# Kernel tuning notes

Measured on AMD Instinct MI355X. Metric: run time of the kernel, lower is better.

## Reference

```python
import jax, jax.numpy as jnp
import numpy as np

B, RES, C = 4, 128, 256
HW = RES * RES
H_FFT, W_FFT = RES, RES // 2 + 1
NUM_BANDS, GATE_HIDDEN = 6, 128
LN_EPS = 1e-5
FFT_NORM = 'ortho'
INIT_RANGE = 0.02


def _band_info(h_fft, w_fft, nb):
    # static radial band partition of the rFFT2 plane (matches RadialBandGate.__init__)
    yy = np.arange(h_fft, dtype=np.float32)[:, None] / max(h_fft - 1, 1)
    xx = np.arange(w_fft, dtype=np.float32)[None, :] / max(w_fft - 1, 1)
    r = np.sqrt(yy ** 2 + xx ** 2)
    r = r / (r.max() + 1e-8)
    bid = np.minimum(np.floor(r * nb), nb - 1).astype(np.int32).reshape(-1)  # (F,)
    onehot = np.zeros((bid.size, nb), dtype=np.float32)
    onehot[np.arange(bid.size), bid] = 1.0
    counts = np.maximum(onehot.sum(0), 1.0)
    return jnp.asarray(bid), jnp.asarray(onehot), jnp.asarray(counts)

BAND_ID, BAND_ONEHOT, BAND_COUNTS = _band_info(H_FFT, W_FFT, NUM_BANDS)


def setup_inputs() -> dict:
    key = jax.random.key(0)
    ks = jax.random.split(key, 16)
    return {
        'x': jax.random.normal(ks[0], (B, HW, C), jnp.float32),
        'time': jax.random.uniform(ks[1], (B,), jnp.float32),
        'w_real': jax.random.normal(ks[2], (C, C), jnp.float32) * INIT_RANGE,
        'w_imag': jax.random.normal(ks[3], (C, C), jnp.float32) * INIT_RANGE,
        'conv_w': jax.random.normal(ks[4], (C, 1, 3, 3), jnp.float32) * 0.1,  # depthwise
        'lin_w': jax.random.normal(ks[5], (C, C), jnp.float32) * 0.02,
        'lin_b': jnp.zeros((C,), jnp.float32),
        'mlp_w1': jax.random.normal(ks[6], (GATE_HIDDEN, NUM_BANDS), jnp.float32) * 0.3,
        'mlp_b1': jnp.zeros((GATE_HIDDEN,), jnp.float32),
        'mlp_w2': jax.random.normal(ks[7], (NUM_BANDS, GATE_HIDDEN), jnp.float32) * 0.1,
        'mlp_b2': jnp.zeros((NUM_BANDS,), jnp.float32),
        'norm_ww': jax.random.normal(ks[8], (C, 1), jnp.float32) * 0.02,  # ConditionalLayerNorm.weight Linear(1,dim)
        'norm_wb': jnp.ones((C,), jnp.float32),
        'norm_bw': jax.random.normal(ks[9], (C, 1), jnp.float32) * 0.02,
        'norm_bb': jnp.zeros((C,), jnp.float32),
        'kx': jnp.asarray(0.25, jnp.float32),
        'ky': jnp.asarray(0.25, jnp.float32),
    }


def _band_gate(feat, mlp_w1, mlp_b1, mlp_w2, mlp_b2):
    # feat: (B, C, F) real. scatter-add per band via one-hot matmul, mean, MLP, gather back.
    sums = jnp.einsum('bcf,fn->bcn', feat, BAND_ONEHOT)           # (B,C,NB)
    means = sums / (BAND_COUNTS + 1e-6)
    h = jax.nn.relu(jnp.einsum('bcn,hn->bch', means, mlp_w1) + mlp_b1)
    alpha_band = jax.nn.sigmoid(jnp.einsum('bch,nh->bcn', h, mlp_w2) + mlp_b2)
    return alpha_band[:, :, BAND_ID]                               # (B,C,F)


def reference(x, time, w_real, w_imag, conv_w, lin_w, lin_b,
              mlp_w1, mlp_b1, mlp_w2, mlp_b2,
              norm_ww, norm_wb, norm_bw, norm_bb, kx, ky):
    h = w = RES
    x2 = jnp.transpose(x.reshape(B, h, w, C), (0, 3, 1, 2))        # (B,C,h,w)
    Xf = jnp.fft.rfft2(x2, norm=FFT_NORM)                          # (B,C,h_fft,w_fft) complex

    # low-frequency rectangular mask (int(sigmoid(k)*dim) == floor for positive values)
    kx_i = jnp.floor(jax.nn.sigmoid(kx) * H_FFT)
    ky_i = jnp.floor(jax.nn.sigmoid(ky) * W_FFT)
    mask = ((jnp.arange(H_FFT)[:, None] < kx_i) & (jnp.arange(W_FFT)[None, :] < ky_i))
    Xf_low = Xf * mask[None, None].astype(Xf.real.dtype)

    F = H_FFT * W_FFT
    Xf_low_flat = Xf_low.reshape(B, C, F)
    W = w_real + 1j * w_imag                                       # (C,C) complex
    Xf_low_mapped = jnp.einsum('cd,bdf->bcf', W, Xf_low_flat).reshape(B, C, H_FFT, W_FFT)

    Xf_high = Xf - Xf_low
    feat_pred = jnp.abs(jnp.abs(Xf_high).reshape(B, C, F) - jnp.abs(Xf_low).reshape(B, C, F))
    alpha = _band_gate(feat_pred, mlp_w1, mlp_b1, mlp_w2, mlp_b2).reshape(B, C, H_FFT, W_FFT)

    Xf_fused = alpha * Xf_low_mapped + (1.0 - alpha) * Xf_high
    x_spec = jnp.fft.irfft2(Xf_fused, s=(h, w), norm=FFT_NORM)     # (B,C,h,w) real

    # depthwise 3x3 conv, padding=1, no bias
    xl = jax.lax.conv_general_dilated(x2, conv_w, window_strides=(1, 1), padding='SAME',
                                      feature_group_count=C,
                                      dimension_numbers=('NCHW', 'OIHW', 'NCHW'))
    # pointwise linear over channel dim
    xc = jnp.transpose((x @ lin_w.T + lin_b).reshape(B, h, w, C), (0, 3, 1, 2))

    y = jnp.transpose(x_spec + xl + xc, (0, 2, 3, 1)).reshape(B, HW, C)

    # ConditionalLayerNorm
    mean = y.mean(axis=-1, keepdims=True)
    var = (y ** 2).mean(axis=-1, keepdims=True) - mean ** 2
    yn = (y - mean) / jnp.sqrt(var + LN_EPS)
    t = time.reshape(-1, 1)                                        # (B,1)
    weight = (t @ norm_ww.T + norm_wb)[:, None, :]                 # (B,1,C)
    bias = (t @ norm_bw.T + norm_bb)[:, None, :]
    return weight * yn + bias
```

## Files before the change

### kernel.cpp

```cpp
#include <hip/hip_runtime.h>
#include <math.h>

#define B_ 4
#define C_ 256
#define RES_ 128
#define HW_ 16384
#define WF_ 65
#define F_ 8320
#define FP_ 2880

typedef __attribute__((ext_vector_type(8))) short bf16x8;
typedef __attribute__((ext_vector_type(16))) float f32x16;

__device__ __forceinline__ int brev6(int j){ return (int)(__brev((unsigned)j) >> 26); }

__device__ __forceinline__ short f2bf(float f){
  unsigned u = __float_as_uint(f);
  unsigned r = (u + 0x7FFFu + ((u>>16)&1u)) >> 16;
  return (short)r;
}

__device__ __forceinline__ bf16x8 lds_frag(const short* p){
  union { bf16x8 v; int2 d[2]; } u;
  u.d[0] = *(const int2*)p;
  u.d[1] = *(const int2*)(p+4);
  return u.v;
}
__device__ __forceinline__ void lds_store8(short* p, bf16x8 v){
  union { bf16x8 v; int2 d[2]; } u; u.v = v;
  *(int2*)p = u.d[0]; *(int2*)(p+4) = u.d[1];
}

__device__ __forceinline__ int band_of(int row, int col){
  float yy = __fdiv_rn((float)row, 127.0f);
  float xx = __fdiv_rn((float)col, 64.0f);
  float rr = __fsqrt_rn(__fadd_rn(__fmul_rn(yy,yy), __fmul_rn(xx,xx)));
  float rm = __fadd_rn(__fsqrt_rn(2.0f), 1e-8f);
  float rn = __fdiv_rn(rr, rm);
  int b = (int)floorf(__fmul_rn(rn, 6.0f));
  return b > 5 ? 5 : b;
}

__device__ __forceinline__ float sigmoidf_(float v){ return 1.0f/(1.0f+expf(-v)); }

template<int SGN>
__device__ __forceinline__ float2 wave_fft64(float2 v, const float2* stw, int lane){
  #pragma unroll
  for (int s=0; s<6; s++){
    int H = 32 >> s;
    float ox = __shfl_xor(v.x, H);
    float oy = __shfl_xor(v.y, H);
    bool hi = (lane & H) != 0;
    float2 w = stw[s];
    float ws = (SGN < 0) ? -w.y : w.y;
    float sx = v.x + ox, sy = v.y + oy;
    float dx = ox - v.x, dy = oy - v.y;
    float rx = dx*w.x - dy*ws;
    float ry = dx*ws + dy*w.x;
    v.x = hi ? rx : sx;
    v.y = hi ? ry : sy;
  }
  return v;
}

__device__ __forceinline__ void make_stage_tw(float2* stw, int lane){
  #pragma unroll
  for (int s=0; s<6; s++){
    int H = 32 >> s;
    int t = (lane & (H-1)) << s;
    float sn, cs;
    sincosf(6.283185307179586f*(float)t/64.0f, &sn, &cs);
    stw[s] = make_float2(cs, sn);
  }
}

__device__ __forceinline__ void redist2(float2 a0, float2 a1, int lane, float2& u0, float2& u1){
  int s0 = lane >> 1, s1 = s0 + 32;
  bool odd = (lane & 1) != 0;
  float t0x = __shfl(a0.x, s0), t0y = __shfl(a0.y, s0);
  float t1x = __shfl(a1.x, s0), t1y = __shfl(a1.y, s0);
  u0 = odd ? make_float2(t1x, t1y) : make_float2(t0x, t0y);
  float q0x = __shfl(a0.x, s1), q0y = __shfl(a0.y, s1);
  float q1x = __shfl(a1.x, s1), q1y = __shfl(a1.y, s1);
  u1 = odd ? make_float2(q1x, q1y) : make_float2(q0x, q0y);
}

__global__ __launch_bounds__(1024) void k_transpose(const float* __restrict__ x, float* __restrict__ x2){
  __shared__ float tile[64][65];
  int b = blockIdx.z;
  int hw0 = blockIdx.x*64, c0 = blockIdx.y*64;
  int tx = threadIdx.x, ty = threadIdx.y;
  #pragma unroll
  for (int i=0;i<4;i++){
    int hw = hw0 + ty + i*16;
    tile[ty+i*16][tx] = x[((size_t)b*HW_ + hw)*C_ + c0 + tx];
  }
  __syncthreads();
  #pragma unroll
  for (int i=0;i<4;i++){
    int c = c0 + ty + i*16;
    x2[((size_t)b*C_ + c)*HW_ + hw0 + tx] = tile[tx][ty+i*16];
  }
}

__global__ __launch_bounds__(256) void k_counts(float* __restrict__ counts, unsigned char* __restrict__ bid_t){
  int tid = threadIdx.x;
  float acc[6] = {0,0,0,0,0,0};
  for (int p = tid; p < F_; p += 256){
    int kx = p >> 7, ky = p & 127;
    int bnd = band_of(ky, kx);
    bid_t[p] = (unsigned char)bnd;
    #pragma unroll
    for (int n=0;n<6;n++) acc[n] += (bnd==n) ? 1.0f : 0.0f;
  }
  __shared__ float red[6][256];
  #pragma unroll
  for (int n=0;n<6;n++) red[n][tid] = acc[n];
  __syncthreads();
  for (int s=128; s>0; s>>=1){
    if (tid < s){
      #pragma unroll
      for (int n=0;n<6;n++) red[n][tid] += red[n][tid+s];
    }
    __syncthreads();
  }
  if (tid < 6) counts[tid] = fmaxf(red[tid][0], 1.0f);
}

__global__ __launch_bounds__(256) void k_wbf16(const float* __restrict__ wre, const float* __restrict__ wim,
                                               const float* __restrict__ lw,
                                               short* __restrict__ Wre, short* __restrict__ Wim,
                                               short* __restrict__ WL){
  int c = blockIdx.x, tid = threadIdx.x, plane = blockIdx.y;
  int idx = c*C_ + tid;
  if (plane == 0)      Wre[idx] = f2bf(wre[idx]);
  else if (plane == 1) Wim[idx] = f2bf(wim[idx]);
  else                 WL[idx]  = f2bf(lw[idx]);
}

__global__ __launch_bounds__(256) void k_fwd_rows(const float* __restrict__ x2, float2* __restrict__ X1t){
  __shared__ float2 tile[65*33];
  int tid = threadIdx.x;
  int lane = tid & 63, wv = tid >> 6;
  float2 stw[6];
  make_stage_tw(stw, lane);
  float sn128, cs128;
  sincosf(6.283185307179586f*(float)lane/128.0f, &sn128, &cs128);
  int slice = blockIdx.x >> 2;
  int r0 = (blockIdx.x & 3) * 32;
  const float* img = x2 + (size_t)slice*HW_ + (size_t)r0*128;
  #pragma unroll
  for (int i=0; i<8; i++){
    int rr = wv*8 + i;
    float2 y = *(const float2*)(img + rr*128 + lane*2);
    float2 v = wave_fft64<-1>(y, stw, lane);
    int rbk = brev6(lane);
    float2 Yk; Yk.x = __shfl(v.x, rbk); Yk.y = __shfl(v.y, rbk);
    int rbm = brev6((64 - lane) & 63);
    float2 Ym; Ym.x = __shfl(v.x, rbm); Ym.y = __shfl(v.y, rbm);
    float sx = Yk.x + Ym.x, sy = Yk.y - Ym.y;
    float dx = Yk.x - Ym.x, dy = Yk.y + Ym.y;
    tile[lane*33 + rr] = make_float2(0.5f*(sx - sn128*dx + cs128*dy),
                                     0.5f*(sy - cs128*dx - sn128*dy));
    if (lane == 0)
      tile[64*33 + rr] = make_float2(Yk.x - Yk.y, 0.0f);
  }
  __syncthreads();
  float2* dst = X1t + (size_t)slice*F_ + r0;
  for (int p = tid; p < 65*32; p += 256){
    int kx = p >> 5, rr = p & 31;
    dst[(size_t)kx*128 + rr] = tile[kx*33 + rr];
  }
}

__global__ __launch_bounds__(256) void k_fwd_cols_gate(const float2* __restrict__ X1t, float2* __restrict__ Xft,
                                                       const float* __restrict__ counts, const unsigned char* __restrict__ bid_t,
                                                       const float* __restrict__ w1, const float* __restrict__ b1,
                                                       const float* __restrict__ w2, const float* __restrict__ b2,
                                                       float* __restrict__ alpha){
  __shared__ float red[6][256];
  __shared__ float means[6], h[128];
  int tid = threadIdx.x;
  int lane = tid & 63, wv = tid >> 6;
  float2 stw[6];
  make_stage_tw(stw, lane);
  float sn128, cs128;
  sincosf(6.283185307179586f*(float)lane/128.0f, &sn128, &cs128);
  int slice = blockIdx.x;
  const float2* xin = X1t + (size_t)slice*F_;
  float2* xout = Xft + (size_t)slice*F_;
  float acc[6] = {0,0,0,0,0,0};
  for (int kx = wv; kx < 65; kx += 4){
    float4 rv = *(const float4*)(xin + (size_t)kx*128 + (lane<<1));
    float2 a0 = make_float2(rv.x, rv.y), a1 = make_float2(rv.z, rv.w);
    float2 u0, u1;
    redist2(a0, a1, lane, u0, u1);
    float2 s = make_float2(u0.x+u1.x, u0.y+u1.y);
    float ddx = u0.x-u1.x, ddy = u0.y-u1.y;
    float2 dw = make_float2(ddx*cs128 + ddy*sn128, ddy*cs128 - ddx*sn128);
    float2 v0 = wave_fft64<-1>(s, stw, lane);
    float2 v1 = wave_fft64<-1>(dw, stw, lane);
    int rb = brev6(lane);
    float ex = __shfl(v0.x, rb), ey = __shfl(v0.y, rb);
    float ox = __shfl(v1.x, rb), oy = __shfl(v1.y, rb);
    ex *= 0.0078125f; ey *= 0.0078125f;
    ox *= 0.0078125f; oy *= 0.0078125f;
    float4 wvout = make_float4(ex, ey, ox, oy);
    *(float4*)(xout + (size_t)kx*128 + (lane<<1)) = wvout;
    float me = __fsqrt_rn(ex*ex + ey*ey);
    float mo = __fsqrt_rn(ox*ox + oy*oy);
    int be = (int)bid_t[kx*128 + (lane<<1)];
    int bo = (int)bid_t[kx*128 + (lane<<1) + 1];
    #pragma unroll
    for (int n=0;n<6;n++) acc[n] += ((be==n) ? me : 0.0f) + ((bo==n) ? mo : 0.0f);
  }
  #pragma unroll
  for (int n=0;n<6;n++) red[n][tid] = acc[n];
  __syncthreads();
  for (int s=128; s>0; s>>=1){
    if (tid < s){
      #pragma unroll
      for (int n=0;n<6;n++) red[n][tid] += red[n][tid+s];
    }
    __syncthreads();
  }
  if (tid < 6) means[tid] = red[tid][0] / (counts[tid] + 1e-6f);
  __syncthreads();
  if (tid < 128){
    float hv = b1[tid];
    #pragma unroll
    for (int n=0;n<6;n++) hv += means[n]*w1[tid*6+n];
    h[tid] = fmaxf(hv, 0.0f);
  }
  __syncthreads();
  if (tid < 6){
    float o = b2[tid];
    for (int j=0;j<128;j++) o += h[j]*w2[tid*128+j];
    alpha[slice*6 + tid] = sigmoidf_(o);
  }
}

__global__ __launch_bounds__(256) void k_xt(const float2* __restrict__ Xft,
                                            short* __restrict__ XtRe, short* __restrict__ XtIm){
  __shared__ short sre[72*130];
  __shared__ short sim[72*130];
  int tid = threadIdx.x;
  int kx = blockIdx.x, d0 = blockIdx.y*128, b = blockIdx.z;
  const float2* xb = Xft + ((size_t)(b*C_ + d0))*F_ + (size_t)kx*128;
  for (int p = tid; p < 72*128; p += 256){
    int d = p / 72, ky = p - d*72;
    float2 v = xb[(size_t)d*F_ + ky];
    sre[ky*130 + d] = f2bf(v.x);
    sim[ky*130 + d] = f2bf(v.y);
  }
  __syncthreads();
  short* dre = XtRe + ((size_t)b*FP_ + (size_t)kx*72)*C_ + d0;
  short* dim_ = XtIm + ((size_t)b*FP_ + (size_t)kx*72)*C_ + d0;
  for (int p = tid; p < 72*128; p += 256){
    int ky = p >> 7, d = p & 127;
    dre[(size_t)ky*C_ + d] = sre[ky*130 + d];
    dim_[(size_t)ky*C_ + d] = sim[ky*130 + d];
  }
}

__global__ __launch_bounds__(256) void k_mix_mfma(const short* __restrict__ Wre, const short* __restrict__ Wim,
                                                  const short* __restrict__ XtRe, const short* __restrict__ XtIm,
                                                  const float* __restrict__ kxp, const float* __restrict__ kyp,
                                                  float2* __restrict__ mappedP){
  __shared__ short Are[64][36], Aim[64][36], Bre[64][36], Bim[64][36];
  int tid = threadIdx.x;
  int fp0 = blockIdx.x*64, c0 = blockIdx.y*64, b = blockIdx.z;
  int lane = tid & 63, w = tid >> 6;
  int mt = (w >> 1)*32, nt = (w & 1)*32;
  f32x16 accre = {0.f,0.f,0.f,0.f,0.f,0.f,0.f,0.f,0.f,0.f,0.f,0.f,0.f,0.f,0.f,0.f};
  f32x16 accim = {0.f,0.f,0.f,0.f,0.f,0.f,0.f,0.f,0.f,0.f,0.f,0.f,0.f,0.f,0.f,0.f};
  const short* xrb = XtRe + ((size_t)b*FP_ + fp0)*C_;
  const short* xib = XtIm + ((size_t)b*FP_ + fp0)*C_;
  int row4 = tid >> 2, part = tid & 3;
  for (int kc=0; kc<8; kc++){
    int d0 = kc*32;
    __syncthreads();
    lds_store8(&Are[row4][part*8], *(const bf16x8*)&Wre[(c0+row4)*C_ + d0 + part*8]);
    lds_store8(&Aim[row4][part*8], *(const bf16x8*)&Wim[(c0+row4)*C_ + d0 + part*8]);
    lds_store8(&Bre[row4][part*8], *(const bf16x8*)&xrb[(size_t)row4*C_ + d0 + part*8]);
    lds_store8(&Bim[row4][part*8], *(const bf16x8*)&xib[(size_t)row4*C_ + d0 + part*8]);
    __syncthreads();
    #pragma unroll
    for (int ks=0; ks<2; ks++){
      int koff = ks*16 + (lane>>5)*8;
      bf16x8 are = lds_frag(&Are[mt + (lane&31)][koff]);
      bf16x8 aim = lds_frag(&Aim[mt + (lane&31)][koff]);
      bf16x8 bre = lds_frag(&Bre[nt + (lane&31)][koff]);
      bf16x8 bim = lds_frag(&Bim[nt + (lane&31)][koff]);
      bf16x8 naim;
      { union { bf16x8 v; unsigned u[4]; } t1, t2; t1.v = aim;
        #pragma unroll
        for (int j=0;j<4;j++) t2.u[j] = t1.u[j] ^ 0x80008000u;
        naim = t2.v; }
      accre = __builtin_amdgcn_mfma_f32_32x32x16_bf16(are,  bre, accre, 0,0,0);
      accre = __builtin_amdgcn_mfma_f32_32x32x16_bf16(naim, bim, accre, 0,0,0);
      accim = __builtin_amdgcn_mfma_f32_32x32x16_bf16(are,  bim, accim, 0,0,0);
      accim = __builtin_amdgcn_mfma_f32_32x32x16_bf16(aim,  bre, accim, 0,0,0);
    }
  }
  float rowlim = floorf(sigmoidf_(kxp[0])*128.0f);
  float collim = floorf(sigmoidf_(kyp[0])*65.0f);
  int n = fp0 + nt + (lane & 31);
  int ky = n % 72, kx = n / 72;
  bool live = ((float)ky < rowlim) && ((float)kx < collim);
  #pragma unroll
  for (int reg=0; reg<16; reg++){
    int r = (reg & 3) + 8*(reg >> 2) + 4*(lane >> 5);
    int c = c0 + mt + r;
    if (live)
      mappedP[((size_t)(b*C_ + c))*FP_ + n] = make_float2(accre[reg], accim[reg]);
  }
}

__global__ __launch_bounds__(256) void k_pw_mfma(const float* __restrict__ x, const short* __restrict__ WL,
                                                  const float* __restrict__ lb, float* __restrict__ xcs){
  __shared__ short As[64][36], Bs[64][36];
  int tid = threadIdx.x;
  int hw0 = blockIdx.x*64, c0 = blockIdx.y*64, b = blockIdx.z;
  int lane = tid & 63, w = tid >> 6;
  int mt = (w >> 1)*32, nt = (w & 1)*32;
  f32x16 acc = {0.f,0.f,0.f,0.f,0.f,0.f,0.f,0.f,0.f,0.f,0.f,0.f,0.f,0.f,0.f,0.f};
  const float* xb = x + ((size_t)b*HW_ + hw0)*C_;
  int row4 = tid >> 2, part = tid & 3;
  for (int kc=0; kc<8; kc++){
    int d0 = kc*32;
    __syncthreads();
    lds_store8(&As[row4][part*8], *(const bf16x8*)&WL[(c0+row4)*C_ + d0 + part*8]);
    {
      const float* src = &xb[(size_t)row4*C_ + d0 + part*8];
      float4 va = *(const float4*)src;
      float4 vb = *(const float4*)(src+4);
      bf16x8 bv;
      bv[0]=f2bf(va.x); bv[1]=f2bf(va.y); bv[2]=f2bf(va.z); bv[3]=f2bf(va.w);
      bv[4]=f2bf(vb.x); bv[5]=f2bf(vb.y); bv[6]=f2bf(vb.z); bv[7]=f2bf(vb.w);
      lds_store8(&Bs[row4][part*8], bv);
    }
    __syncthreads();
    #pragma unroll
    for (int ks=0; ks<2; ks++){
      int koff = ks*16 + (lane>>5)*8;
      bf16x8 a  = lds_frag(&As[mt + (lane&31)][koff]);
      bf16x8 bb = lds_frag(&Bs[nt + (lane&31)][koff]);
      acc = __builtin_amdgcn_mfma_f32_32x32x16_bf16(a, bb, acc, 0,0,0);
    }
  }
  int n = hw0 + nt + (lane & 31);
  #pragma unroll
  for (int reg=0; reg<16; reg++){
    int r = (reg & 3) + 8*(reg >> 2) + 4*(lane >> 5);
    int c = c0 + mt + r;
    xcs[((size_t)(b*C_ + c))*HW_ + n] = acc[reg] + lb[c];
  }
}

__global__ __launch_bounds__(256) void k_inv_cols(float2* __restrict__ XftY, const float2* __restrict__ mappedP,
                                                  const float* __restrict__ alpha, const unsigned char* __restrict__ bid_t,
                                                  const float* __restrict__ kxp, const float* __restrict__ kyp){
  __shared__ float al[6];
  int tid = threadIdx.x;
  int lane = tid & 63, wv = tid >> 6;
  int slice = blockIdx.x;
  float2 stw[6];
  make_stage_tw(stw, lane);
  float sn128, cs128;
  sincosf(6.283185307179586f*(float)lane/128.0f, &sn128, &cs128);
  if (tid < 6) al[tid] = alpha[slice*6 + tid];
  float rowlim = floorf(sigmoidf_(kxp[0])*128.0f);
  float collim = floorf(sigmoidf_(kyp[0])*65.0f);
  __syncthreads();
  float2* xfb = XftY + (size_t)slice*F_;
  const float2* mpb = mappedP + (size_t)slice*FP_;
  for (int kx = wv; kx < 65; kx += 4){
    float4 rv = *(const float4*)(xfb + (size_t)kx*128 + (lane<<1));
    int ky0 = lane << 1;
    float a_e = al[(int)bid_t[kx*128 + ky0]];
    float a_o = al[(int)bid_t[kx*128 + ky0 + 1]];
    bool cok  = ((float)kx < collim);
    bool in_e = cok && ((float)ky0 < rowlim);
    bool in_o = cok && ((float)(ky0+1) < rowlim);
    float2 ve, vo;
    if (in_e){
      float4 mv = *(const float4*)(mpb + (size_t)kx*72 + ky0);
      ve = make_float2(mv.x*a_e, mv.y*a_e);
      vo = in_o ? make_float2(mv.z*a_o, mv.w*a_o)
                : make_float2(rv.z*(1.0f-a_o), rv.w*(1.0f-a_o));
    } else {
      ve = make_float2(rv.x*(1.0f-a_e), rv.y*(1.0f-a_e));
      vo = make_float2(rv.z*(1.0f-a_o), rv.w*(1.0f-a_o));
    }
    float2 u0, u1;
    redist2(ve, vo, lane, u0, u1);
    float2 s = make_float2(u0.x+u1.x, u0.y+u1.y);
    float ddx = u0.x-u1.x, ddy = u0.y-u1.y;
    float2 dw = make_float2(ddx*cs128 - ddy*sn128, ddx*sn128 + ddy*cs128);
    float2 v0 = wave_fft64<1>(s, stw, lane);
    float2 v1 = wave_fft64<1>(dw, stw, lane);
    int rb = brev6(lane);
    float4 outv;
    outv.x = __shfl(v0.x, rb); outv.y = __shfl(v0.y, rb);
    outv.z = __shfl(v1.x, rb); outv.w = __shfl(v1.y, rb);
    *(float4*)(xfb + (size_t)kx*128 + (lane<<1)) = outv;
  }
}

__global__ __launch_bounds__(256,6) void k_inv_rows(const float2* __restrict__ Y1t, const float* __restrict__ xcs,
                                                    const float* __restrict__ x2, const float* __restrict__ cw,
                                                    float* __restrict__ sbuf){
  __shared__ float2 ytile[65*33];
  int tid = threadIdx.x;
  int lane = tid & 63, wv = tid >> 6;
  float2 stw[6];
  make_stage_tw(stw, lane);
  float sn128, cs128;
  sincosf(6.283185307179586f*(float)lane/128.0f, &sn128, &cs128);
  int slice = blockIdx.x >> 2;
  int ch = slice & 255;
  int r0 = (blockIdx.x & 3) * 32;
  const float* img = x2 + (size_t)slice*HW_;
  int base = r0 + wv*8;
  float2 rows[10];
  #pragma unroll
  for (int i=0;i<10;i++){
    int gr = base - 1 + i;
    rows[i] = ((unsigned)gr < 128u) ? *(const float2*)(img + (size_t)gr*128 + (lane<<1))
                                    : make_float2(0.0f, 0.0f);
  }
  const float2* ysrc = Y1t + (size_t)slice*F_ + r0;
  for (int p = tid; p < 65*32; p += 256){
    int kx = p >> 5, rr = p & 31;
    ytile[kx*33 + rr] = ysrc[(size_t)kx*128 + rr];
  }
  float w9[9];
  #pragma unroll
  for (int k=0;k<9;k++) w9[k] = cw[ch*9+k];
  __syncthreads();
  size_t gbase = (size_t)slice*HW_ + (size_t)r0*128;
  #pragma unroll
  for (int i=0;i<8;i++){
    int row = wv*8 + i;
    float2 a = ytile[lane*33 + row];
    float2 b = ytile[(64-lane)*33 + row];
    if (lane == 0){ a.y = 0.0f; b.y = 0.0f; }
    float sx = a.x + b.x, sy = a.y - b.y;
    float dx = a.x - b.x, dy = a.y + b.y;
    float2 yk = make_float2(0.5f*(sx - sn128*dx - cs128*dy),
                            0.5f*(sy + cs128*dx - sn128*dy));
    float2 v = wave_fft64<1>(yk, stw, lane);
    int rbk = brev6(lane);
    float2 z; z.x = __shfl(v.x, rbk); z.y = __shfl(v.y, rbk);
    int xx = lane << 1;
    float c0 = 0.0f, c1 = 0.0f;
    #pragma unroll
    for (int dy2=0; dy2<3; dy2++){
      float2 cv = rows[i + dy2];
      float l = __shfl_up(cv.y, 1);
      if (lane == 0) l = 0.0f;
      float r = __shfl_down(cv.x, 1);
      if (lane == 63) r = 0.0f;
      c0 += l*w9[dy2*3+0] + cv.x*w9[dy2*3+1] + cv.y*w9[dy2*3+2];
      c1 += cv.x*w9[dy2*3+0] + cv.y*w9[dy2*3+1] + r*w9[dy2*3+2];
    }
    size_t g = gbase + (size_t)(row*128 + xx);
    float2 xc = *(const float2*)&xcs[g];
    float2 o;
    o.x = z.x*0.015625f + xc.x + c0;
    o.y = z.y*0.015625f + xc.y + c1;
    *(float2*)&sbuf[g] = o;
  }
}

__global__ __launch_bounds__(256) void k_stats(const float* __restrict__ sbuf, float* __restrict__ stats){
  int g = blockIdx.x*256 + threadIdx.x;
  int b = g >> 14, hw = g & 16383;
  const float* p = sbuf + (size_t)b*C_*HW_ + hw;
  float s1 = 0.0f, s2 = 0.0f;
  for (int c=0; c<C_; c++){
    float v = p[(size_t)c*HW_];
    s1 += v; s2 += v*v;
  }
  float mean = s1 * (1.0f/256.0f);
  float var  = s2 * (1.0f/256.0f) - mean*mean;
  stats[g] = mean;
  stats[65536 + g] = 1.0f / sqrtf(var + 1e-5f);
}

__global__ __launch_bounds__(256) void k_apply(const float* __restrict__ sbuf, const float* __restrict__ stats,
                                               const float* __restrict__ timev,
                                               const float* __restrict__ nww, const float* __restrict__ nwb,
                                               const float* __restrict__ nbw, const float* __restrict__ nbb,
                                               float* __restrict__ out){
  __shared__ float tile[64][65];
  __shared__ float wv[64], bv[64], mv[64], rv[64];
  int b = blockIdx.z, c0 = blockIdx.y*64, hw0 = blockIdx.x*64;
  int tid = threadIdx.x;
  if (tid < 64){
    float t = timev[b];
    int c = c0 + tid;
    wv[tid] = t*nww[c] + nwb[c];
    bv[tid] = t*nbw[c] + nbb[c];
    mv[tid] = stats[(b<<14) + hw0 + tid];
    rv[tid] = stats[65536 + (b<<14) + hw0 + tid];
  }
  #pragma unroll
  for (int q=0;q<16;q++){
    int p = tid + q*256;
    int cl = p >> 6, hwl = p & 63;
    tile[cl][hwl] = sbuf[((size_t)(b*C_+c0+cl))*HW_ + hw0 + hwl];
  }
  __syncthreads();
  #pragma unroll
  for (int q=0;q<16;q++){
    int p = tid + q*256;
    int hwl = p >> 6, cl = p & 63;
    float v = tile[cl][hwl];
    out[((size_t)(b*HW_+hw0+hwl))*C_ + c0 + cl] = wv[cl]*((v - mv[hwl])*rv[hwl]) + bv[cl];
  }
}

extern "C" void kernel_launch(void* const* d_in, const int* in_sizes, int n_in,
                              void* d_out, int out_size, void* d_ws, size_t ws_size,
                              hipStream_t stream){
  const float* x      = (const float*)d_in[0];
  const float* timev  = (const float*)d_in[1];
  const float* w_real = (const float*)d_in[2];
  const float* w_imag = (const float*)d_in[3];
  const float* conv_w = (const float*)d_in[4];
  const float* lin_w  = (const float*)d_in[5];
  const float* lin_b  = (const float*)d_in[6];
  const float* mlp_w1 = (const float*)d_in[7];
  const float* mlp_b1 = (const float*)d_in[8];
  const float* mlp_w2 = (const float*)d_in[9];
  const float* mlp_b2 = (const float*)d_in[10];
  const float* norm_ww= (const float*)d_in[11];
  const float* norm_wb= (const float*)d_in[12];
  const float* norm_bw= (const float*)d_in[13];
  const float* norm_bb= (const float*)d_in[14];
  const float* kxp    = (const float*)d_in[15];
  const float* kyp    = (const float*)d_in[16];

  float* ws = (float*)d_ws;
  float*  alpha  = ws;
  unsigned char* bid_t = (unsigned char*)(ws + 6144);
  float*  counts = ws + 8224;
  float*  stats  = ws + 8288;
  short*  Wre_bf = (short*)(ws + 139360);
  short*  Wim_bf = (short*)(ws + 172128);
  short*  WL_bf  = (short*)(ws + 204896);
  float*  x2     = ws + 237664;
  float2* Xft    = (float2*)(ws + 17014880);
  float*  CbF    = ws + 34054240;
  float2* X1t    = (float2*)CbF;
  short*  XtRe   = (short*)CbF;
  short*  XtIm   = (short*)(CbF + 1474560);
  float2* mappedP= (float2*)(CbF + 2949120);
  float*  sb     = CbF;
  float*  xcs    = (float*)d_out;
  float*  out    = (float*)d_out;

  k_transpose    <<<dim3(256, 4, B_), dim3(64,16), 0, stream>>>(x, x2);
  k_counts       <<<1, 256, 0, stream>>>(counts, bid_t);
  k_wbf16        <<<dim3(256, 3), 256, 0, stream>>>(w_real, w_imag, lin_w, Wre_bf, Wim_bf, WL_bf);
  k_fwd_rows     <<<4096, 256, 0, stream>>>(x2, X1t);
  k_fwd_cols_gate<<<1024, 256, 0, stream>>>(X1t, Xft, counts, bid_t, mlp_w1, mlp_b1, mlp_w2, mlp_b2, alpha);
  k_xt           <<<dim3(40, 2, B_), 256, 0, stream>>>(Xft, XtRe, XtIm);
  k_pw_mfma      <<<dim3(256, 4, B_), 256, 0, stream>>>(x, WL_bf, lin_b, xcs);
  k_mix_mfma     <<<dim3(45, 4, B_), 256, 0, stream>>>(Wre_bf, Wim_bf, XtRe, XtIm, kxp, kyp, mappedP);
  k_inv_cols     <<<1024, 256, 0, stream>>>(Xft, mappedP, alpha, bid_t, kxp, kyp);
  k_inv_rows     <<<4096, 256, 0, stream>>>((const float2*)Xft, xcs, x2, conv_w, sb);
  k_stats        <<<256, 256, 0, stream>>>(sb, stats);
  k_apply        <<<dim3(256, 4, B_), 256, 0, stream>>>(sb, stats, timev, norm_ww, norm_wb, norm_bw, norm_bb, out);
}
```

Measured before the change: 430.6 us.

## Fuse LayerNorm stats into apply, vectorize transposes, warp-reduce gate sums

```diff
diff --git a/kernel.cpp b/kernel.cpp
--- a/kernel.cpp
+++ b/kernel.cpp
@@ -85,21 +85,25 @@
   u1 = odd ? make_float2(q1x, q1y) : make_float2(q0x, q0y);
 }
 
-__global__ __launch_bounds__(1024) void k_transpose(const float* __restrict__ x, float* __restrict__ x2){
-  __shared__ float tile[64][65];
+__global__ __launch_bounds__(256) void k_transpose(const float* __restrict__ x, float* __restrict__ x2){
+  __shared__ float tile[64][68];
   int b = blockIdx.z;
   int hw0 = blockIdx.x*64, c0 = blockIdx.y*64;
-  int tx = threadIdx.x, ty = threadIdx.y;
-  #pragma unroll
-  for (int i=0;i<4;i++){
-    int hw = hw0 + ty + i*16;
-    tile[ty+i*16][tx] = x[((size_t)b*HW_ + hw)*C_ + c0 + tx];
-  }
-  __syncthreads();
-  #pragma unroll
-  for (int i=0;i<4;i++){
-    int c = c0 + ty + i*16;
-    x2[((size_t)b*C_ + c)*HW_ + hw0 + tx] = tile[tx][ty+i*16];
+  int tid = threadIdx.x;
+  #pragma unroll
+  for (int q=0;q<4;q++){
+    int p = tid + q*256;
+    int hw = p >> 4, c4 = (p & 15) << 2;
+    float4 v = *(const float4*)&x[((size_t)b*HW_ + hw0 + hw)*C_ + c0 + c4];
+    *(float4*)&tile[hw][c4] = v;
+  }
+  __syncthreads();
+  #pragma unroll
+  for (int q=0;q<4;q++){
+    int p = tid + q*256;
+    int c = p >> 4, h4 = (p & 15) << 2;
+    float4 v = make_float4(tile[h4][c], tile[h4+1][c], tile[h4+2][c], tile[h4+3][c]);
+    *(float4*)&x2[((size_t)b*C_ + c0 + c)*HW_ + hw0 + h4] = v;
   }
 }
 
@@ -167,9 +171,10 @@
   }
   __syncthreads();
   float2* dst = X1t + (size_t)slice*F_ + r0;
-  for (int p = tid; p < 65*32; p += 256){
-    int kx = p >> 5, rr = p & 31;
-    dst[(size_t)kx*128 + rr] = tile[kx*33 + rr];
+  for (int p = tid; p < 65*16; p += 256){
+    int kx = p >> 4, r2 = (p & 15) << 1;
+    float2 a = tile[kx*33 + r2], b = tile[kx*33 + r2 + 1];
+    *(float4*)(dst + (size_t)kx*128 + r2) = make_float4(a.x, a.y, b.x, b.y);
   }
 }
 
@@ -178,7 +183,7 @@
                                                        const float* __restrict__ w1, const float* __restrict__ b1,
                                                        const float* __restrict__ w2, const float* __restrict__ b2,
                                                        float* __restrict__ alpha){
-  __shared__ float red[6][256];
+  __shared__ float red[6][4];
   __shared__ float means[6], h[128];
   int tid = threadIdx.x;
   int lane = tid & 63, wv = tid >> 6;
@@ -215,16 +220,14 @@
     for (int n=0;n<6;n++) acc[n] += ((be==n) ? me : 0.0f) + ((bo==n) ? mo : 0.0f);
   }
   #pragma unroll
-  for (int n=0;n<6;n++) red[n][tid] = acc[n];
-  __syncthreads();
-  for (int s=128; s>0; s>>=1){
-    if (tid < s){
-      #pragma unroll
-      for (int n=0;n<6;n++) red[n][tid] += red[n][tid+s];
-    }
-    __syncthreads();
-  }
-  if (tid < 6) means[tid] = red[tid][0] / (counts[tid] + 1e-6f);
+  for (int n=0;n<6;n++){
+    float v = acc[n];
+    #pragma unroll
+    for (int off=32; off>0; off>>=1) v += __shfl_xor(v, off);
+    if (lane == 0) red[n][wv] = v;
+  }
+  __syncthreads();
+  if (tid < 6) means[tid] = (red[tid][0]+red[tid][1]+red[tid][2]+red[tid][3]) / (counts[tid] + 1e-6f);
   __syncthreads();
   if (tid < 128){
     float hv = b1[tid];
@@ -408,7 +411,7 @@
   }
 }
 
-__global__ __launch_bounds__(256,6) void k_inv_rows(const float2* __restrict__ Y1t, const float* __restrict__ xcs,
+__global__ __launch_bounds__(256,8) void k_inv_rows(const float2* __restrict__ Y1t, const float* __restrict__ xcs,
                                                     const float* __restrict__ x2, const float* __restrict__ cw,
                                                     float* __restrict__ sbuf){
   __shared__ float2 ytile[65*33];
@@ -431,9 +434,11 @@
                                     : make_float2(0.0f, 0.0f);
   }
   const float2* ysrc = Y1t + (size_t)slice*F_ + r0;
-  for (int p = tid; p < 65*32; p += 256){
-    int kx = p >> 5, rr = p & 31;
-    ytile[kx*33 + rr] = ysrc[(size_t)kx*128 + rr];
+  for (int p = tid; p < 65*16; p += 256){
+    int kx = p >> 4, r2 = (p & 15) << 1;
+    float4 v = *(const float4*)(ysrc + (size_t)kx*128 + r2);
+    ytile[kx*33 + r2]     = make_float2(v.x, v.y);
+    ytile[kx*33 + r2 + 1] = make_float2(v.z, v.w);
   }
   float w9[9];
   #pragma unroll
@@ -474,51 +479,55 @@
   }
 }
 
-__global__ __launch_bounds__(256) void k_stats(const float* __restrict__ sbuf, float* __restrict__ stats){
-  int g = blockIdx.x*256 + threadIdx.x;
-  int b = g >> 14, hw = g & 16383;
-  const float* p = sbuf + (size_t)b*C_*HW_ + hw;
+__global__ __launch_bounds__(256) void k_norm(const float* __restrict__ sbuf, const float* __restrict__ timev,
+                                              const float* __restrict__ nww, const float* __restrict__ nwb,
+                                              const float* __restrict__ nbw, const float* __restrict__ nbb,
+                                              float* __restrict__ out){
+  __shared__ float tile[64][65];
+  __shared__ float p1[64][5], p2[64][5];
+  __shared__ float mv[64], rv[64], wv_[256], bv_[256];
+  int b = blockIdx.y, hw0 = blockIdx.x*64;
+  int tid = threadIdx.x;
+  {
+    float t = timev[b];
+    wv_[tid] = t*nww[tid] + nwb[tid];
+    bv_[tid] = t*nbw[tid] + nbb[tid];
+  }
+  int hwl = tid & 63, cg = tid >> 6;
+  const float* p = sbuf + (size_t)b*C_*HW_ + hw0 + hwl;
   float s1 = 0.0f, s2 = 0.0f;
-  for (int c=0; c<C_; c++){
+  for (int c = cg*64; c < cg*64 + 64; c++){
     float v = p[(size_t)c*HW_];
     s1 += v; s2 += v*v;
   }
-  float mean = s1 * (1.0f/256.0f);
-  float var  = s2 * (1.0f/256.0f) - mean*mean;
-  stats[g] = mean;
-  stats[65536 + g] = 1.0f / sqrtf(var + 1e-5f);
-}
-
-__global__ __launch_bounds__(256) void k_apply(const float* __restrict__ sbuf, const float* __restrict__ stats,
-                                               const float* __restrict__ timev,
-                                               const float* __restrict__ nww, const float* __restrict__ nwb,
-                                               const float* __restrict__ nbw, const float* __restrict__ nbb,
-                                               float* __restrict__ out){
-  __shared__ float tile[64][65];
-  __shared__ float wv[64], bv[64], mv[64], rv[64];
-  int b = blockIdx.z, c0 = blockIdx.y*64, hw0 = blockIdx.x*64;
-  int tid = threadIdx.x;
+  p1[hwl][cg] = s1; p2[hwl][cg] = s2;
+  __syncthreads();
   if (tid < 64){
-    float t = timev[b];
-    int c = c0 + tid;
-    wv[tid] = t*nww[c] + nwb[c];
-    bv[tid] = t*nbw[c] + nbb[c];
-    mv[tid] = stats[(b<<14) + hw0 + tid];
-    rv[tid] = stats[65536 + (b<<14) + hw0 + tid];
-  }
-  #pragma unroll
-  for (int q=0;q<16;q++){
-    int p = tid + q*256;
-    int cl = p >> 6, hwl = p & 63;
-    tile[cl][hwl] = sbuf[((size_t)(b*C_+c0+cl))*HW_ + hw0 + hwl];
-  }
-  __syncthreads();
-  #pragma unroll
-  for (int q=0;q<16;q++){
-    int p = tid + q*256;
-    int hwl = p >> 6, cl = p & 63;
-    float v = tile[cl][hwl];
-    out[((size_t)(b*HW_+hw0+hwl))*C_ + c0 + cl] = wv[cl]*((v - mv[hwl])*rv[hwl]) + bv[cl];
+    float t1 = p1[tid][0] + p1[tid][1] + p1[tid][2] + p1[tid][3];
+    float t2 = p2[tid][0] + p2[tid][1] + p2[tid][2] + p2[tid][3];
+    float mean = t1 * (1.0f/256.0f);
+    float var  = t2 * (1.0f/256.0f) - mean*mean;
+    mv[tid] = mean;
+    rv[tid] = 1.0f / sqrtf(var + 1e-5f);
+  }
+  __syncthreads();
+  for (int cg2=0; cg2<4; cg2++){
+    int c0 = cg2*64;
+    #pragma unroll
+    for (int q=0;q<16;q++){
+      int pp = tid + q*256;
+      int cl = pp >> 6, hl = pp & 63;
+      tile[cl][hl] = sbuf[((size_t)(b*C_ + c0 + cl))*HW_ + hw0 + hl];
+    }
+    __syncthreads();
+    #pragma unroll
+    for (int q=0;q<16;q++){
+      int pp = tid + q*256;
+      int hl = pp >> 6, cl = pp & 63;
+      float v = tile[cl][hl];
+      out[((size_t)(b*HW_ + hw0 + hl))*C_ + c0 + cl] = wv_[c0+cl]*((v - mv[hl])*rv[hl]) + bv_[c0+cl];
+    }
+    __syncthreads();
   }
 }
 
@@ -547,7 +556,6 @@
   float*  alpha  = ws;
   unsigned char* bid_t = (unsigned char*)(ws + 6144);
   float*  counts = ws + 8224;
-  float*  stats  = ws + 8288;
   short*  Wre_bf = (short*)(ws + 139360);
   short*  Wim_bf = (short*)(ws + 172128);
   short*  WL_bf  = (short*)(ws + 204896);
@@ -562,7 +570,7 @@
   float*  xcs    = (float*)d_out;
   float*  out    = (float*)d_out;
 
-  k_transpose    <<<dim3(256, 4, B_), dim3(64,16), 0, stream>>>(x, x2);
+  k_transpose    <<<dim3(256, 4, B_), 256, 0, stream>>>(x, x2);
   k_counts       <<<1, 256, 0, stream>>>(counts, bid_t);
   k_wbf16        <<<dim3(256, 3), 256, 0, stream>>>(w_real, w_imag, lin_w, Wre_bf, Wim_bf, WL_bf);
   k_fwd_rows     <<<4096, 256, 0, stream>>>(x2, X1t);
@@ -572,6 +580,5 @@
   k_mix_mfma     <<<dim3(45, 4, B_), 256, 0, stream>>>(Wre_bf, Wim_bf, XtRe, XtIm, kxp, kyp, mappedP);
   k_inv_cols     <<<1024, 256, 0, stream>>>(Xft, mappedP, alpha, bid_t, kxp, kyp);
   k_inv_rows     <<<4096, 256, 0, stream>>>((const float2*)Xft, xcs, x2, conv_w, sb);
-  k_stats        <<<256, 256, 0, stream>>>(sb, stats);
-  k_apply        <<<dim3(256, 4, B_), 256, 0, stream>>>(sb, stats, timev, norm_ww, norm_wb, norm_bw, norm_bb, out);
-}
+  k_norm         <<<dim3(256, B_), 256, 0, stream>>>(sb, timev, norm_ww, norm_wb, norm_bw, norm_bb, out);
+}
```

After: 438.8 us. About the same (+1.9%).
